# Performance work log

Measured on AMD Instinct MI355X. Metric: run time of the kernel, lower is better.

Reference implementation:

```python
import jax, jax.numpy as jnp
import numpy as np

N_NODES = 100000
N_EDGES = 50000
NNZ = 1600000
D_IN = 128
D_OUT = 128  # heads(8) * out_channels(16)


def setup_inputs() -> dict:
    key = jax.random.key(0)
    k1, k2, k3, k4 = jax.random.split(key, 4)
    X = jax.random.normal(k1, (N_NODES, D_IN), dtype=jnp.float32)
    W = jax.random.normal(k2, (D_IN, D_OUT), dtype=jnp.float32) * (1.0 / np.sqrt(D_IN))
    eps = jnp.zeros((1,), dtype=jnp.float32)
    vertex = jax.random.randint(k3, (NNZ,), 0, N_NODES, dtype=jnp.int32)
    edges = jax.random.randint(k4, (NNZ,), 0, N_EDGES, dtype=jnp.int32)
    return {"X": X, "W": W, "eps": eps, "vertex": vertex, "edges": edges,
            "num_edges": N_EDGES}


def reference(X, W, eps, vertex, edges, num_edges):
    N = X.shape[0]
    Xp = X @ W                                   # [N, D_OUT] linear proj (no bias)
    Xve = Xp[vertex]                             # [nnz, D_OUT] vertex -> incidence gather
    Xe = jax.ops.segment_sum(Xve, edges, num_segments=num_edges)   # [E, D_OUT] first_aggregate='sum'
    Xev = Xe[edges]                              # [nnz, D_OUT] edge -> incidence gather
    Xv = jax.ops.segment_sum(Xev, vertex, num_segments=N)          # [N, D_OUT]
    out = (1.0 + eps) * Xp + Xv                  # GIN combine with learnable eps (eps is [1], broadcasts)
    return jax.nn.gelu(out, approximate=False)   # torch F.gelu default = exact erf
```

## Files before the change

### kernel.cpp

```cpp
#include <hip/hip_runtime.h>
#include <math.h>

#define NN 100000
#define NE 50000
#define NSEG (NE + NN)
#define DD 128

#define NBE 196
#define NBV 391
#define NB  (NBE + NBV)
#define CAP_E 8960
#define CAP_V 4608

typedef short bf16x8 __attribute__((ext_vector_type(8)));
typedef float f32x4 __attribute__((ext_vector_type(4)));
typedef float v2f __attribute__((ext_vector_type(2)));

static __device__ __forceinline__ float gelu_exact(float x) {
  return 0.5f * x * (1.0f + erff(x * 0.70710678118654752f));
}

static __device__ __forceinline__ int bucket_base(int g) {
  return (g < NBE) ? g * CAP_E : NBE * CAP_E + (g - NBE) * CAP_V;
}

static __device__ __forceinline__ void acc2(v2f& a, unsigned u) {
  union { unsigned i; float f; } lo, hi;
  lo.i = u << 16;
  hi.i = u & 0xFFFF0000u;
  v2f t;
  t.x = lo.f;
  t.y = hi.f;
  a += t;
}

static __device__ __forceinline__ unsigned pack_bf16x2(float a, float b) {
  unsigned ua = __float_as_uint(a), ub = __float_as_uint(b);
  ua = (ua + 0x7FFFu + ((ua >> 16) & 1u)) >> 16;
  ub = (ub + 0x7FFFu + ((ub >> 16) & 1u)) >> 16;
  return ua | (ub << 16);
}

static __device__ __forceinline__ unsigned short bf16_rne(float a) {
  unsigned ua = __float_as_uint(a);
  ua = (ua + 0x7FFFu + ((ua >> 16) & 1u)) >> 16;
  return (unsigned short)ua;
}

__global__ __launch_bounds__(256) void k_init(int* __restrict__ gcur,
                                              const float* __restrict__ W,
                                              unsigned short* __restrict__ Wt) {
  const int b = blockIdx.x;
  if (b < 64) {
    int idx = b * 256 + threadIdx.x;
    int k = idx >> 7, n = idx & 127;
    Wt[n * 128 + k] = bf16_rne(W[idx]);
  } else {
    int g = (b - 64) * 256 + threadIdx.x;
    if (g < NB) gcur[g] = bucket_base(g);
  }
}

__global__ __launch_bounds__(256) void k_gemm(const float* __restrict__ X,
                                              const unsigned short* __restrict__ Wt,
                                              unsigned short* __restrict__ Xb2) {
  const int tid = threadIdx.x;
  const int w = tid >> 6;
  const int l = tid & 63;
  const int lm = l & 15;
  const int lk = l >> 4;
  const int R = blockIdx.x * 64 + w * 16;
  const int arow = R + lm;
  const bool rowok = arow < NN;
  const f32x4* __restrict__ X4 = (const f32x4*)X;
  const uint4* __restrict__ Wt4 = (const uint4*)Wt;

  f32x4 acc[8];
#pragma unroll
  for (int t = 0; t < 8; ++t) acc[t] = (f32x4)(0.f);

  for (int c = 0; c < 4; ++c) {
    const int k0 = c * 32 + lk * 8;
    f32x4 x0 = (f32x4)(0.f), x1 = (f32x4)(0.f);
    if (rowok) {
      x0 = __builtin_nontemporal_load(&X4[arow * 32 + (k0 >> 2)]);
      x1 = __builtin_nontemporal_load(&X4[arow * 32 + (k0 >> 2) + 1]);
    }
    union { bf16x8 v; uint4 u; } a;
    a.u.x = pack_bf16x2(x0.x, x0.y);
    a.u.y = pack_bf16x2(x0.z, x0.w);
    a.u.z = pack_bf16x2(x1.x, x1.y);
    a.u.w = pack_bf16x2(x1.z, x1.w);
#pragma unroll
    for (int t = 0; t < 8; ++t) {
      union { bf16x8 v; uint4 u; } b;
      b.u = Wt4[(t * 16 + lm) * 16 + c * 4 + lk];
      acc[t] = __builtin_amdgcn_mfma_f32_16x16x32_bf16(a.v, b.v, acc[t], 0, 0, 0);
    }
  }

  const int drow = R + lk * 4;
#pragma unroll
  for (int r = 0; r < 4; ++r) {
    const int row = drow + r;
    if (row < NN) {
#pragma unroll
      for (int t = 0; t < 8; ++t) {
        Xb2[row * 128 + t * 16 + lm] = bf16_rne(acc[t][r]);
      }
    }
  }
}

__global__ __launch_bounds__(256) void k_pass1(const int* __restrict__ vertex,
                                               const int* __restrict__ edges,
                                               int* __restrict__ gcur,
                                               int* __restrict__ S, int nnz) {
  __shared__ int hist[NB];
  const int tid = threadIdx.x;
  for (int b = tid; b < NB; b += 256) hist[b] = 0;
  __syncthreads();
  const int base = blockIdx.x * 4096;
#pragma unroll
  for (int k = 0; k < 16; ++k) {
    int i = base + tid + k * 256;
    if (i < nnz) {
      atomicAdd(&hist[edges[i] >> 8], 1);
      atomicAdd(&hist[NBE + (vertex[i] >> 8)], 1);
    }
  }
  __syncthreads();
  for (int b = tid; b < NB; b += 256) {
    int c = hist[b];
    hist[b] = c ? atomicAdd(&gcur[b], c) : 0;
  }
  __syncthreads();
#pragma unroll
  for (int k = 0; k < 16; ++k) {
    int i = base + tid + k * 256;
    if (i < nnz) {
      int e = edges[i], v = vertex[i];
      int pe = atomicAdd(&hist[e >> 8], 1);
      S[pe] = ((e & 255) << 17) | v;
      int pv = atomicAdd(&hist[NBE + (v >> 8)], 1);
      S[pv] = ((v & 255) << 17) | e;
    }
  }
}

__global__ __launch_bounds__(256) void k_pass2(const int* __restrict__ gcur,
                                               const int* __restrict__ S,
                                               int* __restrict__ L,
                                               int* __restrict__ O) {
  __shared__ int offs[257];
  __shared__ int cur[256];
  __shared__ int scratch[CAP_E];
  const int g = blockIdx.x;
  const int tid = threadIdx.x;
  int part = 0;
  for (int i = tid; i < g; i += 256) part += gcur[i] - bucket_base(i);
  cur[tid] = part;
  __syncthreads();
#pragma unroll
  for (int s2 = 128; s2 > 0; s2 >>= 1) {
    if (tid < s2) cur[tid] += cur[tid + s2];
    __syncthreads();
  }
  const int dbase = cur[0];
  __syncthreads();

  const bool isE = g < NBE;
  const int sstart = bucket_base(g);
  int nit = gcur[g] - sstart;
  const int cap = isE ? CAP_E : CAP_V;
  if (nit > cap) nit = cap;
  const int s0 = isE ? (g << 8) : ((g - NBE) << 8);
  const int segN = min(256, (isE ? NE : NN) - s0);
  const int obase = isE ? s0 : NE + s0;
  for (int k = tid; k < 257; k += 256) offs[k] = 0;
  __syncthreads();
  for (int t = tid; t < nit; t += 256) atomicAdd(&offs[(S[sstart + t] >> 17) + 1], 1);
  __syncthreads();
  for (int off = 1; off < 256; off <<= 1) {
    int y = (tid >= off) ? offs[tid + 1 - off] : 0;
    __syncthreads();
    offs[tid + 1] += y;
    __syncthreads();
  }
  cur[tid] = offs[tid];
  __syncthreads();
  for (int t = tid; t < nit; t += 256) {
    int u = S[sstart + t];
    int r = atomicAdd(&cur[u >> 17], 1);
    scratch[r] = u & 0x1FFFF;
  }
  __syncthreads();
  for (int t = tid; t < nit; t += 256) L[dbase + t] = scratch[t];
  for (int k = tid; k <= segN; k += 256) O[obase + k] = dbase + offs[k];
}

__global__ __launch_bounds__(256) void k_edge_agg(const unsigned* __restrict__ Xb2,
                                                  const int* __restrict__ O,
                                                  const int* __restrict__ L,
                                                  unsigned* __restrict__ Xe2) {
  const int e = blockIdx.x * 4 + (threadIdx.x >> 6);
  const int lane = threadIdx.x & 63;
  const int q = lane >> 4;
  const int ql = lane & 15;
  const int start = O[e];
  const int end = O[e + 1];
  const uint4* __restrict__ P = (const uint4*)Xb2;
  v2f a[4];
#pragma unroll
  for (int k = 0; k < 4; ++k) a[k] = (v2f)(0.f);
  int j = start + q;
  for (; j + 12 < end; j += 16) {
    uint4 u0 = P[L[j] * 16 + ql];
    uint4 u1 = P[L[j + 4] * 16 + ql];
    uint4 u2 = P[L[j + 8] * 16 + ql];
    uint4 u3 = P[L[j + 12] * 16 + ql];
    acc2(a[0], u0.x); acc2(a[1], u0.y); acc2(a[2], u0.z); acc2(a[3], u0.w);
    acc2(a[0], u1.x); acc2(a[1], u1.y); acc2(a[2], u1.z); acc2(a[3], u1.w);
    acc2(a[0], u2.x); acc2(a[1], u2.y); acc2(a[2], u2.z); acc2(a[3], u2.w);
    acc2(a[0], u3.x); acc2(a[1], u3.y); acc2(a[2], u3.z); acc2(a[3], u3.w);
  }
  if (j + 4 < end) {
    uint4 u0 = P[L[j] * 16 + ql];
    uint4 u1 = P[L[j + 4] * 16 + ql];
    acc2(a[0], u0.x); acc2(a[1], u0.y); acc2(a[2], u0.z); acc2(a[3], u0.w);
    acc2(a[0], u1.x); acc2(a[1], u1.y); acc2(a[2], u1.z); acc2(a[3], u1.w);
    j += 8;
  }
  if (j < end) {
    uint4 u0 = P[L[j] * 16 + ql];
    acc2(a[0], u0.x); acc2(a[1], u0.y); acc2(a[2], u0.z); acc2(a[3], u0.w);
  }
#pragma unroll
  for (int k = 0; k < 4; ++k) {
    float u0 = a[k].x, u1 = a[k].y;
    u0 += __shfl_xor(u0, 16); u0 += __shfl_xor(u0, 32);
    u1 += __shfl_xor(u1, 16); u1 += __shfl_xor(u1, 32);
    a[k].x = u0; a[k].y = u1;
  }
  float s0 = (q == 0) ? a[0].x : (q == 1) ? a[1].x : (q == 2) ? a[2].x : a[3].x;
  float s1 = (q == 0) ? a[0].y : (q == 1) ? a[1].y : (q == 2) ? a[2].y : a[3].y;
  Xe2[e * 64 + ql * 4 + q] = pack_bf16x2(s0, s1);
}

__global__ __launch_bounds__(256) void k_vert_agg(const unsigned* __restrict__ Xe2,
                                                  const int* __restrict__ O,
                                                  const int* __restrict__ L,
                                                  const float* __restrict__ eps,
                                                  const unsigned* __restrict__ Xb2,
                                                  float* __restrict__ out) {
  const int v = blockIdx.x * 4 + (threadIdx.x >> 6);
  const int lane = threadIdx.x & 63;
  const int q = lane >> 4;
  const int ql = lane & 15;
  const int start = O[NE + v];
  const int end = O[NE + v + 1];
  const uint4* __restrict__ Q = (const uint4*)Xe2;
  v2f a[4];
#pragma unroll
  for (int k = 0; k < 4; ++k) a[k] = (v2f)(0.f);
  int j = start + q;
  for (; j + 12 < end; j += 16) {
    uint4 u0 = Q[L[j] * 16 + ql];
    uint4 u1 = Q[L[j + 4] * 16 + ql];
    uint4 u2 = Q[L[j + 8] * 16 + ql];
    uint4 u3 = Q[L[j + 12] * 16 + ql];
    acc2(a[0], u0.x); acc2(a[1], u0.y); acc2(a[2], u0.z); acc2(a[3], u0.w);
    acc2(a[0], u1.x); acc2(a[1], u1.y); acc2(a[2], u1.z); acc2(a[3], u1.w);
    acc2(a[0], u2.x); acc2(a[1], u2.y); acc2(a[2], u2.z); acc2(a[3], u2.w);
    acc2(a[0], u3.x); acc2(a[1], u3.y); acc2(a[2], u3.z); acc2(a[3], u3.w);
  }
  if (j + 4 < end) {
    uint4 u0 = Q[L[j] * 16 + ql];
    uint4 u1 = Q[L[j + 4] * 16 + ql];
    acc2(a[0], u0.x); acc2(a[1], u0.y); acc2(a[2], u0.z); acc2(a[3], u0.w);
    acc2(a[0], u1.x); acc2(a[1], u1.y); acc2(a[2], u1.z); acc2(a[3], u1.w);
    j += 8;
  }
  if (j < end) {
    uint4 u0 = Q[L[j] * 16 + ql];
    acc2(a[0], u0.x); acc2(a[1], u0.y); acc2(a[2], u0.z); acc2(a[3], u0.w);
  }
#pragma unroll
  for (int k = 0; k < 4; ++k) {
    float u0 = a[k].x, u1 = a[k].y;
    u0 += __shfl_xor(u0, 16); u0 += __shfl_xor(u0, 32);
    u1 += __shfl_xor(u1, 16); u1 += __shfl_xor(u1, 32);
    a[k].x = u0; a[k].y = u1;
  }
  float s0 = (q == 0) ? a[0].x : (q == 1) ? a[1].x : (q == 2) ? a[2].x : a[3].x;
  float s1 = (q == 0) ? a[0].y : (q == 1) ? a[1].y : (q == 2) ? a[2].y : a[3].y;
  unsigned su = Xb2[v * 64 + ql * 4 + q];
  union { unsigned i; float f; } plo, phi;
  plo.i = su << 16;
  phi.i = su & 0xFFFF0000u;
  const float sc = 1.0f + eps[0];
  v2f x;
  x.x = gelu_exact(fmaf(sc, plo.f, s0));
  x.y = gelu_exact(fmaf(sc, phi.f, s1));
  v2f* __restrict__ P2 = (v2f*)out;
  __builtin_nontemporal_store(x, &P2[v * 64 + ql * 4 + q]);
}

extern "C" void kernel_launch(void* const* d_in, const int* in_sizes, int n_in,
                              void* d_out, int out_size, void* d_ws, size_t ws_size,
                              hipStream_t stream) {
  const float* X = (const float*)d_in[0];
  const float* W = (const float*)d_in[1];
  const float* eps = (const float*)d_in[2];
  const int* vertex = (const int*)d_in[3];
  const int* edges = (const int*)d_in[4];
  const int nnz = in_sizes[3];

  char* ws = (char*)d_ws;
  size_t off = 0;
  auto alloc = [&](size_t bytes) -> void* {
    void* p = ws + off;
    off = (off + bytes + 255) & ~(size_t)255;
    return p;
  };
  const size_t stagingB = ((size_t)NBE * CAP_E + (size_t)NBV * CAP_V) * 4;
  const size_t xbB = (size_t)NN * DD * 2;
  void* A = alloc(xbB > stagingB ? xbB : stagingB);
  int* S = (int*)A;
  unsigned short* Xb2 = (unsigned short*)A;
  unsigned* Xe2 = (unsigned*)alloc((size_t)NE * DD * 2);
  int* L = (int*)alloc((size_t)2 * nnz * sizeof(int));
  int* O = (int*)alloc((size_t)(NSEG + 1) * sizeof(int));
  int* gcur = (int*)alloc((size_t)NB * sizeof(int));
  unsigned short* Wt = (unsigned short*)alloc((size_t)DD * DD * 2);
  if (off > ws_size) return;

  k_init<<<67, 256, 0, stream>>>(gcur, W, Wt);
  k_pass1<<<(nnz + 4095) / 4096, 256, 0, stream>>>(vertex, edges, gcur, S, nnz);
  k_pass2<<<NB, 256, 0, stream>>>(gcur, S, L, O);
  k_gemm<<<(NN + 63) / 64, 256, 0, stream>>>(X, Wt, Xb2);
  k_edge_agg<<<NE / 4, 256, 0, stream>>>((const unsigned*)Xb2, O, L, Xe2);
  k_vert_agg<<<NN / 4, 256, 0, stream>>>(Xe2, O, L, eps, (const unsigned*)Xb2,
                                         (float*)d_out);
}
```

Measured before the change: 308.6 us.

## Split feature columns into four chunks and use 16-bit vertex index lists

Projected features and edge aggregates are stored in a column-chunked layout of four 32-wide slices. The edge and vertex aggregation kernels gain a grid dimension over chunks, so each gather touches only one 64-byte slice and the per-chunk working set is more likely to stay in cache. The vertex-side incidence list is stored as 16-bit edge indices to cut index traffic, and the offset arrays are adjusted to fit. In exchange, every index list is re-read four times, each gather is a narrow 4-byte load per lane, and only a quarter of the lanes do the final write.

```diff
diff --git a/kernel.cpp b/kernel.cpp
--- a/kernel.cpp
+++ b/kernel.cpp
@@ -63,7 +63,7 @@
 
 __global__ __launch_bounds__(256) void k_gemm(const float* __restrict__ X,
                                               const unsigned short* __restrict__ Wt,
-                                              unsigned short* __restrict__ Xb2) {
+                                              unsigned short* __restrict__ Xb2c) {
   const int tid = threadIdx.x;
   const int w = tid >> 6;
   const int l = tid & 63;
@@ -106,7 +106,8 @@
     if (row < NN) {
 #pragma unroll
       for (int t = 0; t < 8; ++t) {
-        Xb2[row * 128 + t * 16 + lm] = bf16_rne(acc[t][r]);
+        Xb2c[((size_t)(t >> 1) * NN + row) * 32 + (t & 1) * 16 + lm] =
+            bf16_rne(acc[t][r]);
       }
     }
   }
@@ -150,8 +151,9 @@
 
 __global__ __launch_bounds__(256) void k_pass2(const int* __restrict__ gcur,
                                                const int* __restrict__ S,
-                                               int* __restrict__ L,
-                                               int* __restrict__ O) {
+                                               int* __restrict__ LE,
+                                               unsigned short* __restrict__ LV,
+                                               int* __restrict__ O, int nnz) {
   __shared__ int offs[257];
   __shared__ int cur[256];
   __shared__ int scratch[CAP_E];
@@ -166,17 +168,17 @@
     if (tid < s2) cur[tid] += cur[tid + s2];
     __syncthreads();
   }
-  const int dbase = cur[0];
-  __syncthreads();
-
   const bool isE = g < NBE;
+  const int dbase = isE ? cur[0] : cur[0] - nnz;
+  __syncthreads();
+
   const int sstart = bucket_base(g);
   int nit = gcur[g] - sstart;
   const int cap = isE ? CAP_E : CAP_V;
   if (nit > cap) nit = cap;
   const int s0 = isE ? (g << 8) : ((g - NBE) << 8);
   const int segN = min(256, (isE ? NE : NN) - s0);
-  const int obase = isE ? s0 : NE + s0;
+  const int obase = isE ? s0 : NE + 1 + s0;
   for (int k = tid; k < 257; k += 256) offs[k] = 0;
   __syncthreads();
   for (int t = tid; t < nit; t += 256) atomicAdd(&offs[(S[sstart + t] >> 17) + 1], 1);
@@ -195,115 +197,97 @@
     scratch[r] = u & 0x1FFFF;
   }
   __syncthreads();
-  for (int t = tid; t < nit; t += 256) L[dbase + t] = scratch[t];
+  if (isE) {
+    for (int t = tid; t < nit; t += 256) LE[dbase + t] = scratch[t];
+  } else {
+    for (int t = tid; t < nit; t += 256) LV[dbase + t] = (unsigned short)scratch[t];
+  }
   for (int k = tid; k <= segN; k += 256) O[obase + k] = dbase + offs[k];
 }
 
-__global__ __launch_bounds__(256) void k_edge_agg(const unsigned* __restrict__ Xb2,
+__global__ __launch_bounds__(256) void k_edge_agg(const unsigned* __restrict__ Xb2c,
                                                   const int* __restrict__ O,
-                                                  const int* __restrict__ L,
-                                                  unsigned* __restrict__ Xe2) {
+                                                  const int* __restrict__ LE,
+                                                  unsigned* __restrict__ Xe2c) {
+  const int c = blockIdx.y;
   const int e = blockIdx.x * 4 + (threadIdx.x >> 6);
   const int lane = threadIdx.x & 63;
   const int q = lane >> 4;
   const int ql = lane & 15;
   const int start = O[e];
   const int end = O[e + 1];
-  const uint4* __restrict__ P = (const uint4*)Xb2;
-  v2f a[4];
-#pragma unroll
-  for (int k = 0; k < 4; ++k) a[k] = (v2f)(0.f);
+  const unsigned* __restrict__ P = Xb2c + (size_t)c * NN * 16;
+  v2f a = (v2f)(0.f);
   int j = start + q;
   for (; j + 12 < end; j += 16) {
-    uint4 u0 = P[L[j] * 16 + ql];
-    uint4 u1 = P[L[j + 4] * 16 + ql];
-    uint4 u2 = P[L[j + 8] * 16 + ql];
-    uint4 u3 = P[L[j + 12] * 16 + ql];
-    acc2(a[0], u0.x); acc2(a[1], u0.y); acc2(a[2], u0.z); acc2(a[3], u0.w);
-    acc2(a[0], u1.x); acc2(a[1], u1.y); acc2(a[2], u1.z); acc2(a[3], u1.w);
-    acc2(a[0], u2.x); acc2(a[1], u2.y); acc2(a[2], u2.z); acc2(a[3], u2.w);
-    acc2(a[0], u3.x); acc2(a[1], u3.y); acc2(a[2], u3.z); acc2(a[3], u3.w);
+    unsigned u0 = P[(size_t)LE[j] * 16 + ql];
+    unsigned u1 = P[(size_t)LE[j + 4] * 16 + ql];
+    unsigned u2 = P[(size_t)LE[j + 8] * 16 + ql];
+    unsigned u3 = P[(size_t)LE[j + 12] * 16 + ql];
+    acc2(a, u0); acc2(a, u1); acc2(a, u2); acc2(a, u3);
   }
   if (j + 4 < end) {
-    uint4 u0 = P[L[j] * 16 + ql];
-    uint4 u1 = P[L[j + 4] * 16 + ql];
-    acc2(a[0], u0.x); acc2(a[1], u0.y); acc2(a[2], u0.z); acc2(a[3], u0.w);
-    acc2(a[0], u1.x); acc2(a[1], u1.y); acc2(a[2], u1.z); acc2(a[3], u1.w);
+    unsigned u0 = P[(size_t)LE[j] * 16 + ql];
+    unsigned u1 = P[(size_t)LE[j + 4] * 16 + ql];
+    acc2(a, u0); acc2(a, u1);
     j += 8;
   }
   if (j < end) {
-    uint4 u0 = P[L[j] * 16 + ql];
-    acc2(a[0], u0.x); acc2(a[1], u0.y); acc2(a[2], u0.z); acc2(a[3], u0.w);
-  }
-#pragma unroll
-  for (int k = 0; k < 4; ++k) {
-    float u0 = a[k].x, u1 = a[k].y;
-    u0 += __shfl_xor(u0, 16); u0 += __shfl_xor(u0, 32);
-    u1 += __shfl_xor(u1, 16); u1 += __shfl_xor(u1, 32);
-    a[k].x = u0; a[k].y = u1;
-  }
-  float s0 = (q == 0) ? a[0].x : (q == 1) ? a[1].x : (q == 2) ? a[2].x : a[3].x;
-  float s1 = (q == 0) ? a[0].y : (q == 1) ? a[1].y : (q == 2) ? a[2].y : a[3].y;
-  Xe2[e * 64 + ql * 4 + q] = pack_bf16x2(s0, s1);
-}
-
-__global__ __launch_bounds__(256) void k_vert_agg(const unsigned* __restrict__ Xe2,
+    acc2(a, P[(size_t)LE[j] * 16 + ql]);
+  }
+  a.x += __shfl_xor(a.x, 16); a.x += __shfl_xor(a.x, 32);
+  a.y += __shfl_xor(a.y, 16); a.y += __shfl_xor(a.y, 32);
+  if (q == 0) {
+    Xe2c[((size_t)c * NE + e) * 16 + ql] = pack_bf16x2(a.x, a.y);
+  }
+}
+
+__global__ __launch_bounds__(256) void k_vert_agg(const unsigned* __restrict__ Xe2c,
                                                   const int* __restrict__ O,
-                                                  const int* __restrict__ L,
+                                                  const unsigned short* __restrict__ LV,
                                                   const float* __restrict__ eps,
-                                                  const unsigned* __restrict__ Xb2,
+                                                  const unsigned* __restrict__ Xb2c,
                                                   float* __restrict__ out) {
+  const int c = blockIdx.y;
   const int v = blockIdx.x * 4 + (threadIdx.x >> 6);
   const int lane = threadIdx.x & 63;
   const int q = lane >> 4;
   const int ql = lane & 15;
-  const int start = O[NE + v];
-  const int end = O[NE + v + 1];
-  const uint4* __restrict__ Q = (const uint4*)Xe2;
-  v2f a[4];
-#pragma unroll
-  for (int k = 0; k < 4; ++k) a[k] = (v2f)(0.f);
+  const int start = O[NE + 1 + v];
+  const int end = O[NE + 2 + v];
+  const unsigned* __restrict__ Q = Xe2c + (size_t)c * NE * 16;
+  v2f a = (v2f)(0.f);
   int j = start + q;
   for (; j + 12 < end; j += 16) {
-    uint4 u0 = Q[L[j] * 16 + ql];
-    uint4 u1 = Q[L[j + 4] * 16 + ql];
-    uint4 u2 = Q[L[j + 8] * 16 + ql];
-    uint4 u3 = Q[L[j + 12] * 16 + ql];
-    acc2(a[0], u0.x); acc2(a[1], u0.y); acc2(a[2], u0.z); acc2(a[3], u0.w);
-    acc2(a[0], u1.x); acc2(a[1], u1.y); acc2(a[2], u1.z); acc2(a[3], u1.w);
-    acc2(a[0], u2.x); acc2(a[1], u2.y); acc2(a[2], u2.z); acc2(a[3], u2.w);
-    acc2(a[0], u3.x); acc2(a[1], u3.y); acc2(a[2], u3.z); acc2(a[3], u3.w);
+    unsigned u0 = Q[(size_t)LV[j] * 16 + ql];
+    unsigned u1 = Q[(size_t)LV[j + 4] * 16 + ql];
+    unsigned u2 = Q[(size_t)LV[j + 8] * 16 + ql];
+    unsigned u3 = Q[(size_t)LV[j + 12] * 16 + ql];
+    acc2(a, u0); acc2(a, u1); acc2(a, u2); acc2(a, u3);
   }
   if (j + 4 < end) {
-    uint4 u0 = Q[L[j] * 16 + ql];
-    uint4 u1 = Q[L[j + 4] * 16 + ql];
-    acc2(a[0], u0.x); acc2(a[1], u0.y); acc2(a[2], u0.z); acc2(a[3], u0.w);
-    acc2(a[0], u1.x); acc2(a[1], u1.y); acc2(a[2], u1.z); acc2(a[3], u1.w);
+    unsigned u0 = Q[(size_t)LV[j] * 16 + ql];
+    unsigned u1 = Q[(size_t)LV[j + 4] * 16 + ql];
+    acc2(a, u0); acc2(a, u1);
     j += 8;
   }
   if (j < end) {
-    uint4 u0 = Q[L[j] * 16 + ql];
-    acc2(a[0], u0.x); acc2(a[1], u0.y); acc2(a[2], u0.z); acc2(a[3], u0.w);
-  }
-#pragma unroll
-  for (int k = 0; k < 4; ++k) {
-    float u0 = a[k].x, u1 = a[k].y;
-    u0 += __shfl_xor(u0, 16); u0 += __shfl_xor(u0, 32);
-    u1 += __shfl_xor(u1, 16); u1 += __shfl_xor(u1, 32);
-    a[k].x = u0; a[k].y = u1;
-  }
-  float s0 = (q == 0) ? a[0].x : (q == 1) ? a[1].x : (q == 2) ? a[2].x : a[3].x;
-  float s1 = (q == 0) ? a[0].y : (q == 1) ? a[1].y : (q == 2) ? a[2].y : a[3].y;
-  unsigned su = Xb2[v * 64 + ql * 4 + q];
-  union { unsigned i; float f; } plo, phi;
-  plo.i = su << 16;
-  phi.i = su & 0xFFFF0000u;
-  const float sc = 1.0f + eps[0];
-  v2f x;
-  x.x = gelu_exact(fmaf(sc, plo.f, s0));
-  x.y = gelu_exact(fmaf(sc, phi.f, s1));
-  v2f* __restrict__ P2 = (v2f*)out;
-  __builtin_nontemporal_store(x, &P2[v * 64 + ql * 4 + q]);
+    acc2(a, Q[(size_t)LV[j] * 16 + ql]);
+  }
+  a.x += __shfl_xor(a.x, 16); a.x += __shfl_xor(a.x, 32);
+  a.y += __shfl_xor(a.y, 16); a.y += __shfl_xor(a.y, 32);
+  if (q == 0) {
+    unsigned su = __builtin_nontemporal_load(&Xb2c[((size_t)c * NN + v) * 16 + ql]);
+    union { unsigned i; float f; } plo, phi;
+    plo.i = su << 16;
+    phi.i = su & 0xFFFF0000u;
+    const float sc = 1.0f + eps[0];
+    v2f x;
+    x.x = gelu_exact(fmaf(sc, plo.f, a.x));
+    x.y = gelu_exact(fmaf(sc, phi.f, a.y));
+    v2f* __restrict__ P2 = (v2f*)out;
+    __builtin_nontemporal_store(x, &P2[(size_t)v * 64 + c * 16 + ql]);
+  }
 }
 
 extern "C" void kernel_launch(void* const* d_in, const int* in_sizes, int n_in,
@@ -327,19 +311,21 @@
   const size_t xbB = (size_t)NN * DD * 2;
   void* A = alloc(xbB > stagingB ? xbB : stagingB);
   int* S = (int*)A;
-  unsigned short* Xb2 = (unsigned short*)A;
-  unsigned* Xe2 = (unsigned*)alloc((size_t)NE * DD * 2);
-  int* L = (int*)alloc((size_t)2 * nnz * sizeof(int));
-  int* O = (int*)alloc((size_t)(NSEG + 1) * sizeof(int));
+  unsigned short* Xb2c = (unsigned short*)A;
+  unsigned* Xe2c = (unsigned*)alloc((size_t)NE * DD * 2);
+  int* LE = (int*)alloc((size_t)nnz * sizeof(int));
+  unsigned short* LV =
+      (unsigned short*)alloc((size_t)nnz * sizeof(unsigned short));
+  int* O = (int*)alloc((size_t)(NSEG + 2) * sizeof(int));
   int* gcur = (int*)alloc((size_t)NB * sizeof(int));
   unsigned short* Wt = (unsigned short*)alloc((size_t)DD * DD * 2);
   if (off > ws_size) return;
 
   k_init<<<67, 256, 0, stream>>>(gcur, W, Wt);
   k_pass1<<<(nnz + 4095) / 4096, 256, 0, stream>>>(vertex, edges, gcur, S, nnz);
-  k_pass2<<<NB, 256, 0, stream>>>(gcur, S, L, O);
-  k_gemm<<<(NN + 63) / 64, 256, 0, stream>>>(X, Wt, Xb2);
-  k_edge_agg<<<NE / 4, 256, 0, stream>>>((const unsigned*)Xb2, O, L, Xe2);
-  k_vert_agg<<<NN / 4, 256, 0, stream>>>(Xe2, O, L, eps, (const unsigned*)Xb2,
-                                         (float*)d_out);
-}
+  k_pass2<<<NB, 256, 0, stream>>>(gcur, S, LE, LV, O, nnz);
+  k_gemm<<<(NN + 63) / 64, 256, 0, stream>>>(X, Wt, Xb2c);
+  k_edge_agg<<<dim3(NE / 4, 4), 256, 0, stream>>>((const unsigned*)Xb2c, O, LE, Xe2c);
+  k_vert_agg<<<dim3(NN / 4, 4), 256, 0, stream>>>(Xe2c, O, LV, eps,
+                                                  (const unsigned*)Xb2c, (float*)d_out);
+}
```

Measured after the change: 427.6 us. 38.6% more time.
